# Kernel tuning notes

Hardware: AMD Instinct MI355X
Metric: run time of the kernel (lower is better)

## Reference

```python
import jax, jax.numpy as jnp
import numpy as np

B, S, HID = 2, 2048, 2048
NH, NKV, HD = 16, 4, 128
G = NH // NKV  # kv group size
EPS = 1e-6


def setup_inputs() -> dict:
    key = jax.random.key(0)
    ks = jax.random.split(key, 7)
    w = 0.02
    return {
        "hidden_states": jax.random.normal(ks[0], (B, S, HID), dtype=jnp.float32),
        "position_ids": jnp.broadcast_to(jnp.arange(S, dtype=jnp.int64), (B, S)),
        "Wq": jax.random.normal(ks[1], (2 * NH * HD, HID), dtype=jnp.float32) * w,
        "Wk": jax.random.normal(ks[2], (NKV * HD, HID), dtype=jnp.float32) * w,
        "Wv": jax.random.normal(ks[3], (NKV * HD, HID), dtype=jnp.float32) * w,
        "Wo": jax.random.normal(ks[4], (HID, NH * HD), dtype=jnp.float32) * w,
        "norm_w": jnp.zeros((HID,), dtype=jnp.float32),
    }


def reference(hidden_states, position_ids, Wq, Wk, Wv, Wo, norm_w):
    # RMSNorm (weight parameterized as 1 + w, per source)
    ms = jnp.mean(hidden_states * hidden_states, axis=-1, keepdims=True)
    x = hidden_states * jax.lax.rsqrt(ms + EPS) * (1.0 + norm_w)

    qg = x @ Wq.T                                   # (B,S,2*NH*HD)
    q, gate = jnp.split(qg, 2, axis=-1)
    q = q.reshape(B, S, NH, HD).transpose(0, 2, 1, 3)       # (B,NH,S,HD)
    gate = gate.reshape(B, S, NH, HD).transpose(0, 2, 1, 3)
    k = (x @ Wk.T).reshape(B, S, NKV, HD).transpose(0, 2, 1, 3)  # (B,NKV,S,HD)
    v = (x @ Wv.T).reshape(B, S, NKV, HD).transpose(0, 2, 1, 3)

    scale = 1.0 / np.sqrt(HD).astype(np.float32)
    qg4 = q.reshape(B, NKV, G, S, HD)
    attn = jnp.einsum("bkgqd,bkld->bkgql", qg4, k) * scale   # (B,NKV,G,S,S)
    p = jax.nn.softmax(attn, axis=-1)
    o = jnp.einsum("bkgql,bkld->bkgqd", p, v).reshape(B, NH, S, HD)

    o = o * jax.nn.sigmoid(gate)                    # output gate
    o = o.transpose(0, 2, 1, 3).reshape(B, S, NH * HD)
    return o @ Wo.T
```

## Files before the change

kernel.cpp:

```cpp
#include <hip/hip_runtime.h>
#include <math.h>

#define BB    2
#define SS    2048
#define HIDD  2048
#define NHH   16
#define NKVV  4
#define HDD   128
#define MROWS 4096
#define QG_N  4096
#define KV_N  512
#define O_N   2048
#define KDIM  2048
#define EPS_  1e-6f
#define SCALE_ 0.08838834764831845f
#define SCALE2_ (0.08838834764831845f * 1.4426950408889634f)
#define THR2_  11.5417f
#define NWBLK 14336

typedef __attribute__((ext_vector_type(8))) __bf16 bf16x8;
typedef __attribute__((ext_vector_type(8))) unsigned short u16x8;
typedef __attribute__((ext_vector_type(4))) float f32x4;

__device__ __forceinline__ unsigned short f2bf(float f) {
  return __builtin_bit_cast(unsigned short, (__bf16)f);
}
__device__ __forceinline__ float fexp2(float x) {
  return __builtin_amdgcn_exp2f(x);
}

__global__ __launch_bounds__(256) void prep_k(const float* __restrict__ Wq,
                                              const float* __restrict__ Wk,
                                              const float* __restrict__ Wv,
                                              const float* __restrict__ Wo,
                                              const float* __restrict__ hs,
                                              const float* __restrict__ nw,
                                              unsigned short* __restrict__ wdst,
                                              unsigned short* __restrict__ x) {
  if (blockIdx.x < NWBLK) {
    const int s0 = QG_N * KDIM / 4;
    const int s1 = s0 + KV_N * KDIM / 4;
    const int s2 = s1 + KV_N * KDIM / 4;
    int i = blockIdx.x * 256 + threadIdx.x;
    float4 v;
    if (i < s0)      v = ((const float4*)Wq)[i];
    else if (i < s1) v = ((const float4*)Wk)[i - s0];
    else if (i < s2) v = ((const float4*)Wv)[i - s1];
    else             v = ((const float4*)Wo)[i - s2];
    ushort4 u;
    u.x = f2bf(v.x); u.y = f2bf(v.y); u.z = f2bf(v.z); u.w = f2bf(v.w);
    ((ushort4*)wdst)[i] = u;
    return;
  }
  int row = blockIdx.x - NWBLK;
  int t = threadIdx.x;
  const float4* hr = (const float4*)(hs + (size_t)row * HIDD);
  const float4* w4 = (const float4*)nw;

  float4 v0 = hr[t], v1 = hr[t + 256];
  float ss = v0.x*v0.x + v0.y*v0.y + v0.z*v0.z + v0.w*v0.w
           + v1.x*v1.x + v1.y*v1.y + v1.z*v1.z + v1.w*v1.w;
#pragma unroll
  for (int off = 32; off > 0; off >>= 1) ss += __shfl_down(ss, off, 64);

  __shared__ float part[4];
  __shared__ float rs_sh;
  if ((t & 63) == 0) part[t >> 6] = ss;
  __syncthreads();
  if (t == 0) rs_sh = rsqrtf((part[0]+part[1]+part[2]+part[3]) * (1.0f/HIDD) + EPS_);
  __syncthreads();
  float rs = rs_sh;

  float4 w0 = w4[t], w1 = w4[t + 256];
  ushort4 o0, o1;
  o0.x = f2bf(v0.x * rs * (1.f + w0.x));
  o0.y = f2bf(v0.y * rs * (1.f + w0.y));
  o0.z = f2bf(v0.z * rs * (1.f + w0.z));
  o0.w = f2bf(v0.w * rs * (1.f + w0.w));
  o1.x = f2bf(v1.x * rs * (1.f + w1.x));
  o1.y = f2bf(v1.y * rs * (1.f + w1.y));
  o1.z = f2bf(v1.z * rs * (1.f + w1.z));
  o1.w = f2bf(v1.w * rs * (1.f + w1.w));
  ushort4* xr = (ushort4*)(x + (size_t)row * HIDD);
  xr[t] = o0;
  xr[t + 256] = o1;
}

template <int OBF>
__device__ __forceinline__ void gemm_core(const unsigned short* __restrict__ Ab,
                                          const unsigned short* __restrict__ Bb,
                                          void* __restrict__ Cv,
                                          int Ndim, int bm, int bn,
                                          unsigned short* Als, unsigned short* Bls) {
  char* ldsA = (char*)Als;
  char* ldsB = (char*)Bls;

  int t   = threadIdx.x;
  int r15 = t & 15;
  int g   = (t & 63) >> 4;
  int w   = t >> 6;
  int wr  = w >> 1, wc = w & 1;

  f32x4 acc[4][4] = {};

  for (int k0 = 0; k0 < KDIM; k0 += 64) {
    __syncthreads();
#pragma unroll
    for (int it = 0; it < 4; ++it) {
      int f      = it * 256 + t;
      int row    = f >> 3;
      int schunk = (f & 7) ^ (row & 7);
      unsigned ldsbase = (unsigned)((it * 256 + (w << 6)) << 4);
      __builtin_amdgcn_global_load_lds(
          (const unsigned int*)(Ab + ((size_t)(bm + row) << 11) + k0 + schunk * 8),
          (unsigned int*)(ldsA + ldsbase), 16, 0, 0);
      __builtin_amdgcn_global_load_lds(
          (const unsigned int*)(Bb + ((size_t)(bn + row) << 11) + k0 + schunk * 8),
          (unsigned int*)(ldsB + ldsbase), 16, 0, 0);
    }
    __syncthreads();

#pragma unroll
    for (int tt = 0; tt < 2; ++tt) {
      bf16x8 af[4], bfv[4];
#pragma unroll
      for (int mi = 0; mi < 4; ++mi) {
        int row = wr * 64 + mi * 16 + r15;
        af[mi] = *(const bf16x8*)(ldsA + row * 128 + (((4 * tt + g) ^ (row & 7)) << 4));
      }
#pragma unroll
      for (int ni = 0; ni < 4; ++ni) {
        int row = wc * 64 + ni * 16 + r15;
        bfv[ni] = *(const bf16x8*)(ldsB + row * 128 + (((4 * tt + g) ^ (row & 7)) << 4));
      }
      __builtin_amdgcn_s_setprio(1);
#pragma unroll
      for (int mi = 0; mi < 4; ++mi)
#pragma unroll
        for (int ni = 0; ni < 4; ++ni)
          acc[mi][ni] = __builtin_amdgcn_mfma_f32_16x16x32_bf16(af[mi], bfv[ni], acc[mi][ni], 0, 0, 0);
      __builtin_amdgcn_s_setprio(0);
    }
  }

#pragma unroll
  for (int mi = 0; mi < 4; ++mi)
#pragma unroll
    for (int ni = 0; ni < 4; ++ni) {
      int col = bn + wc * 64 + ni * 16 + r15;
#pragma unroll
      for (int r = 0; r < 4; ++r) {
        int rowg = bm + wr * 64 + mi * 16 + g * 4 + r;
        if (OBF == 1)
          ((unsigned short*)Cv)[(size_t)rowg * Ndim + col] = f2bf(acc[mi][ni][r]);
        else if (OBF == 3) {
          int t6 = rowg & 63;
          int sig = (t6 & 32) + ((t6 & 12) << 1) + ((t6 & 16) >> 2) + (t6 & 3);
          int tokp = (rowg & ~63) | sig;
          ((unsigned short*)Cv)[(size_t)col * MROWS + tokp] = f2bf(acc[mi][ni][r]);
        } else
          ((float*)Cv)[(size_t)rowg * Ndim + col] = acc[mi][ni][r];
      }
    }
}

__global__ __launch_bounds__(256) void gemm_kv(const unsigned short* __restrict__ Ab,
                                               const unsigned short* __restrict__ Wk,
                                               const unsigned short* __restrict__ Wv,
                                               unsigned short* __restrict__ Ck,
                                               unsigned short* __restrict__ Cvt) {
  __shared__ unsigned short Als[128 * 64];
  __shared__ unsigned short Bls[128 * 64];
  int bx = blockIdx.x;
  if (bx < 4)
    gemm_core<1>(Ab, Wk, (void*)Ck, KV_N, blockIdx.y * 128, bx * 128, Als, Bls);
  else
    gemm_core<3>(Ab, Wv, (void*)Cvt, KV_N, blockIdx.y * 128, (bx & 3) * 128, Als, Bls);
}

#define LD8(basep, r, x) \
  (*(const bf16x8*)((basep) + (size_t)(r) * 128 + ((((x) ^ ((r)&7))) << 4)))

#define STAGE_A(bufi, h, tk)                                                   \
  { _Pragma("unroll")                                                          \
    for (int c = 0; c < 2; ++c) {                                              \
      int f = c * 512 + t;                                                     \
      int rr = f >> 3;                                                         \
      int sc = (f & 7) ^ (rr & 7);                                             \
      __builtin_amdgcn_global_load_lds(                                        \
        (const unsigned int*)(Ab + ((size_t)(bm + (h)*128 + rr) << 11) + (tk)*64 + sc*8), \
        (unsigned int*)(lds8 + (bufi)*32768 + (h)*16384 + c*8192 + (w<<10)), 16, 0, 0); \
    } }

#define STAGE_B(bufi, h, tk)                                                   \
  { _Pragma("unroll")                                                          \
    for (int c = 0; c < 2; ++c) {                                              \
      int f = c * 512 + t;                                                     \
      int rr = f >> 3;                                                         \
      int sc = (f & 7) ^ (rr & 7);                                             \
      __builtin_amdgcn_global_load_lds(                                        \
        (const unsigned int*)(Bbp + ((size_t)(bn + (h)*128 + rr) << 11) + (tk)*64 + sc*8), \
        (unsigned int*)(lds8 + 65536 + (bufi)*32768 + (h)*16384 + c*8192 + (w<<10)), 16, 0, 0); \
    } }

#define RD_A(SRC, MIBASE)                                                      \
  { _Pragma("unroll")                                                          \
    for (int mi = 0; mi < 4; ++mi) {                                           \
      int rr = wr * 128 + ((MIBASE) + mi) * 16 + r15;                          \
      afr[mi][0] = LD8(SRC, rr, g);                                            \
      afr[mi][1] = LD8(SRC, rr, 4 + g);                                        \
    } }

#define RD_B(SRC, NIBASE, DST)                                                 \
  { _Pragma("unroll")                                                          \
    for (int ni = 0; ni < 2; ++ni) {                                           \
      int rr = wc * 64 + ((NIBASE) + ni) * 16 + r15;                           \
      DST[ni][0] = LD8(SRC, rr, g);                                            \
      DST[ni][1] = LD8(SRC, rr, 4 + g);                                        \
    } }

#define MFMA_QUAD(MIBASE, NIBASE, BREG)                                        \
  { __builtin_amdgcn_s_setprio(1);                                             \
    _Pragma("unroll")                                                          \
    for (int mi = 0; mi < 4; ++mi)                                             \
      _Pragma("unroll")                                                        \
      for (int ni = 0; ni < 2; ++ni)                                           \
        _Pragma("unroll")                                                      \
        for (int ks = 0; ks < 2; ++ks)                                         \
          acc[(MIBASE)+mi][(NIBASE)+ni] =                                      \
            __builtin_amdgcn_mfma_f32_16x16x32_bf16(afr[mi][ks], BREG[ni][ks], \
                                                    acc[(MIBASE)+mi][(NIBASE)+ni], 0, 0, 0); \
    __builtin_amdgcn_s_setprio(0); }

#define BAR() __builtin_amdgcn_s_barrier()

__global__ __launch_bounds__(512, 2) void gemm_qg256(const unsigned short* __restrict__ Ab,
                                                     const unsigned short* __restrict__ Bbp,
                                                     unsigned short* __restrict__ Cq,
                                                     float* __restrict__ Cg) {
  __shared__ char lds8[131072];
  int t = threadIdx.x;
  int r15 = t & 15, g = (t & 63) >> 4, w = t >> 6;
  int wr = w >> 2, wc = w & 3;
  int bm = blockIdx.y * 256, bn = blockIdx.x * 256;
  char* A0 = lds8;            char* A1 = lds8 + 32768;
  char* B0 = lds8 + 65536;    char* B1 = lds8 + 98304;

  f32x4 acc[8][4] = {};
  bf16x8 afr[4][2], b0r[2][2], b1r[2][2];

  STAGE_A(0, 0, 0); STAGE_A(0, 1, 0); STAGE_B(0, 0, 0); STAGE_B(0, 1, 0);
  STAGE_A(1, 0, 1); STAGE_A(1, 1, 1); STAGE_B(1, 0, 1); STAGE_B(1, 1, 1);
  asm volatile("s_waitcnt vmcnt(8)" ::: "memory");
  BAR();

  for (int i = 0; i < 15; ++i) {
    int te = 2 * i + 2, to = 2 * i + 3;
    RD_A(A0, 0); RD_B(B0, 0, b0r);
    BAR(); MFMA_QUAD(0, 0, b0r); BAR();
    RD_B(B0, 2, b1r);
    BAR(); MFMA_QUAD(0, 2, b1r); BAR();
    RD_A(A0, 4);
    STAGE_B(0, 0, te);
    BAR(); MFMA_QUAD(4, 0, b0r); BAR();
    STAGE_A(0, 0, te);
    BAR(); MFMA_QUAD(4, 2, b1r);
    asm volatile("s_waitcnt vmcnt(4)" ::: "memory");
    BAR();
    RD_A(A1, 0); RD_B(B1, 0, b0r);
    STAGE_A(0, 1, te);
    BAR(); MFMA_QUAD(0, 0, b0r); BAR();
    RD_B(B1, 2, b1r);
    STAGE_B(0, 1, te);
    BAR(); MFMA_QUAD(0, 2, b1r); BAR();
    RD_A(A1, 4);
    STAGE_B(1, 0, to); STAGE_B(1, 1, to);
    BAR(); MFMA_QUAD(4, 0, b0r); BAR();
    STAGE_A(1, 0, to); STAGE_A(1, 1, to);
    BAR(); MFMA_QUAD(4, 2, b1r);
    asm volatile("s_waitcnt vmcnt(8)" ::: "memory");
    BAR();
  }
  RD_A(A0, 0); RD_B(B0, 0, b0r);
  BAR(); MFMA_QUAD(0, 0, b0r); BAR();
  RD_B(B0, 2, b1r);
  BAR(); MFMA_QUAD(0, 2, b1r); BAR();
  RD_A(A0, 4);
  BAR(); MFMA_QUAD(4, 0, b0r); BAR();
  BAR(); MFMA_QUAD(4, 2, b1r);
  asm volatile("s_waitcnt vmcnt(0)" ::: "memory");
  BAR();
  RD_A(A1, 0); RD_B(B1, 0, b0r);
  BAR(); MFMA_QUAD(0, 0, b0r); BAR();
  RD_B(B1, 2, b1r);
  BAR(); MFMA_QUAD(0, 2, b1r); BAR();
  RD_A(A1, 4);
  BAR(); MFMA_QUAD(4, 0, b0r); BAR();
  BAR(); MFMA_QUAD(4, 2, b1r);

  bool isq = (bn < O_N);
  int colbase = bn + wc * 64;
#pragma unroll
  for (int mi = 0; mi < 8; ++mi) {
    size_t row = (size_t)bm + wr * 128 + mi * 16 + g * 4;
#pragma unroll
    for (int ni = 0; ni < 4; ++ni) {
      int col = colbase + ni * 16 + r15;
#pragma unroll
      for (int r = 0; r < 4; ++r) {
        if (isq) Cq[(row + r) * O_N + col] = f2bf(acc[mi][ni][r] * SCALE2_);
        else     Cg[(row + r) * O_N + (col - O_N)] = acc[mi][ni][r];
      }
    }
  }
}

#define OST_A(bufi, h, tk)                                                     \
  { _Pragma("unroll")                                                          \
    for (int c = 0; c < 2; ++c) {                                              \
      int f = c * 512 + t;                                                     \
      int rr = f >> 3;                                                         \
      int sc = (f & 7) ^ (rr & 7);                                             \
      __builtin_amdgcn_global_load_lds(                                        \
        (const unsigned int*)(Ab + ((size_t)(bm + (h)*128 + rr) << 11) + (tk)*64 + sc*8), \
        (unsigned int*)(lds8 + (bufi)*32768 + (h)*16384 + c*8192 + (w<<10)), 16, 0, 0); \
    } }

#define OST_B(bufi, tk)                                                        \
  { _Pragma("unroll")                                                          \
    for (int c = 0; c < 2; ++c) {                                              \
      int f = c * 512 + t;                                                     \
      int rr = f >> 3;                                                         \
      int sc = (f & 7) ^ (rr & 7);                                             \
      __builtin_amdgcn_global_load_lds(                                        \
        (const unsigned int*)(Bbp + ((size_t)(bn + rr) << 11) + (tk)*64 + sc*8), \
        (unsigned int*)(lds8 + 65536 + (bufi)*16384 + c*8192 + (w<<10)), 16, 0, 0); \
    } }

#define ORD_A(bufi)                                                            \
  { const char* abase = lds8 + (bufi)*32768 + (wr >> 1)*16384;                 \
    _Pragma("unroll")                                                          \
    for (int mi = 0; mi < 4; ++mi) {                                           \
      int rl = ((wr & 1) * 64) + mi * 16 + r15;                                \
      afr[mi][0] = LD8(abase, rl, g);                                          \
      afr[mi][1] = LD8(abase, rl, 4 + g);                                      \
    } }

#define ORD_B(bufi, NIBASE, DST)                                               \
  { const char* bbase = lds8 + 65536 + (bufi)*16384;                           \
    _Pragma("unroll")                                                          \
    for (int ni = 0; ni < 2; ++ni) {                                           \
      int rl = wc * 64 + ((NIBASE) + ni) * 16 + r15;                           \
      DST[ni][0] = LD8(bbase, rl, g);                                          \
      DST[ni][1] = LD8(bbase, rl, 4 + g);                                      \
    } }

#define OMFMA(NIBASE, BREG)                                                    \
  { __builtin_amdgcn_s_setprio(1);                                             \
    _Pragma("unroll")                                                          \
    for (int mi = 0; mi < 4; ++mi)                                             \
      _Pragma("unroll")                                                        \
      for (int ni = 0; ni < 2; ++ni)                                           \
        _Pragma("unroll")                                                      \
        for (int ks = 0; ks < 2; ++ks)                                         \
          acc[mi][(NIBASE)+ni] =                                               \
            __builtin_amdgcn_mfma_f32_16x16x32_bf16(afr[mi][ks], BREG[ni][ks], \
                                                    acc[mi][(NIBASE)+ni], 0, 0, 0); \
    __builtin_amdgcn_s_setprio(0); }

__global__ __launch_bounds__(512, 2) void gemm_o256(const unsigned short* __restrict__ Ab,
                                                    const unsigned short* __restrict__ Bbp,
                                                    float* __restrict__ C) {
  __shared__ char lds8[98304];
  int t = threadIdx.x;
  int r15 = t & 15, g = (t & 63) >> 4, w = t >> 6;
  int wr = w >> 1, wc = w & 1;
  int bm = blockIdx.y * 256, bn = blockIdx.x * 128;

  f32x4 acc[4][4] = {};
  bf16x8 afr[4][2], b0r[2][2], b1r[2][2];

  OST_A(0, 0, 0); OST_A(0, 1, 0); OST_B(0, 0);
  OST_A(1, 0, 1); OST_A(1, 1, 1);
  asm volatile("s_waitcnt vmcnt(4)" ::: "memory");
  BAR();

  for (int i = 0; i < 15; ++i) {
    int to = 2 * i + 1, te2 = 2 * i + 2, to2 = 2 * i + 3;
    ORD_A(0); ORD_B(0, 0, b0r);
    OST_B(1, to);
    BAR(); OMFMA(0, b0r); BAR();
    ORD_B(0, 2, b1r);
    OST_A(0, 0, te2);
    BAR(); OMFMA(2, b1r);
    asm volatile("s_waitcnt vmcnt(2)" ::: "memory");
    BAR();
    ORD_A(1); ORD_B(1, 0, b0r);
    OST_A(0, 1, te2); OST_B(0, te2);
    BAR(); OMFMA(0, b0r); BAR();
    ORD_B(1, 2, b1r);
    OST_A(1, 0, to2); OST_A(1, 1, to2);
    BAR(); OMFMA(2, b1r);
    asm volatile("s_waitcnt vmcnt(4)" ::: "memory");
    BAR();
  }
  ORD_A(0); ORD_B(0, 0, b0r);
  OST_B(1, 31);
  BAR(); OMFMA(0, b0r); BAR();
  ORD_B(0, 2, b1r);
  BAR(); OMFMA(2, b1r);
  asm volatile("s_waitcnt vmcnt(0)" ::: "memory");
  BAR();
  ORD_A(1); ORD_B(1, 0, b0r);
  BAR(); OMFMA(0, b0r); BAR();
  ORD_B(1, 2, b1r);
  BAR(); OMFMA(2, b1r);

#pragma unroll
  for (int mi = 0; mi < 4; ++mi) {
    size_t row = (size_t)bm + wr * 64 + mi * 16 + g * 4;
#pragma unroll
    for (int ni = 0; ni < 4; ++ni) {
      int col = bn + wc * 64 + ni * 16 + r15;
#pragma unroll
      for (int r = 0; r < 4; ++r)
        C[(row + r) * O_N + col] = acc[mi][ni][r];
    }
  }
}

__global__ __launch_bounds__(256, 2) void attn_mfma(const unsigned short* __restrict__ qb,
                                                    const float* __restrict__ gateb,
                                                    const unsigned short* __restrict__ kb,
                                                    const unsigned short* __restrict__ vt,
                                                    unsigned short* __restrict__ obuf) {
  __shared__ unsigned short Ks[2][64 * 128];
  __shared__ unsigned short Vt[2][128 * 64];
  char* ldsK0 = (char*)Ks;
  char* ldsV0 = (char*)Vt;

  int t = threadIdx.x;
  int l = t & 63, w = t >> 6;
  int c15 = l & 15, g = l >> 4;
  int bid = blockIdx.x;
  int swz = (bid & 7) * 64 + (bid >> 3);
  int qt = swz & 15, h = (swz >> 4) & 15, b = swz >> 8;
  int kh = h >> 2;
  size_t rowQ0 = (size_t)b * SS + (size_t)qt * 128;
  size_t rowKbase = (size_t)b * SS;

  bf16x8 qf[2][4];
#pragma unroll
  for (int qi = 0; qi < 2; ++qi)
#pragma unroll
    for (int ks = 0; ks < 4; ++ks)
      qf[qi][ks] = *(const bf16x8*)(qb + (rowQ0 + w * 32 + qi * 16 + c15) * O_N
                                       + h * HDD + g * 8 + ks * 32);

  f32x4 accO[2][8] = {};
  float mrun[2] = {-INFINITY, -INFINITY};
  float lrun[2] = {0.f, 0.f};

#define ISSUE_K(bufi, kt_)                                                     \
  {                                                                            \
    size_t rowK0 = rowKbase + (size_t)(kt_) * 64;                              \
    _Pragma("unroll")                                                          \
    for (int it = 0; it < 4; ++it) {                                           \
      int f = it * 256 + t;                                                    \
      int kv = f >> 4;                                                         \
      int schunk = (f & 15) ^ (kv & 7);                                        \
      unsigned ldsbase = (unsigned)((it * 256 + (w << 6)) << 4);               \
      __builtin_amdgcn_global_load_lds(                                        \
          (const unsigned int*)(kb + (rowK0 + kv) * KV_N + kh * HDD + schunk * 8), \
          (unsigned int*)(ldsK0 + (bufi) * 16384 + ldsbase), 16, 0, 0);        \
    }                                                                          \
  }
#define ISSUE_VT(bufi, kt_)                                                    \
  {                                                                            \
    size_t tokbase = rowKbase + (size_t)(kt_) * 64;                            \
    _Pragma("unroll")                                                          \
    for (int it = 0; it < 4; ++it) {                                           \
      int f = it * 256 + t;                                                    \
      int row = f >> 3;                                                        \
      int schunk = (f & 7) ^ (row & 7);                                        \
      unsigned ldsbase = (unsigned)((it * 256 + (w << 6)) << 4);               \
      __builtin_amdgcn_global_load_lds(                                        \
          (const unsigned int*)(vt + (size_t)(kh * 128 + row) * MROWS + tokbase + schunk * 8), \
          (unsigned int*)(ldsV0 + (bufi) * 16384 + ldsbase), 16, 0, 0);        \
    }                                                                          \
  }

  ISSUE_K(0, 0);
  ISSUE_VT(0, 0);
  asm volatile("s_waitcnt vmcnt(0)" ::: "memory");
  __syncthreads();

  const int NT = SS / 64;
  for (int kt = 0; kt < NT; ++kt) {
    int cur = kt & 1, nxt = cur ^ 1;
    char* ldsK = ldsK0 + cur * 16384;
    char* ldsV = ldsV0 + cur * 16384;

    if (kt + 1 < NT) {
      ISSUE_K(nxt, kt + 1);
      ISSUE_VT(nxt, kt + 1);
    }

    f32x4 accS[2][4] = {};
    __builtin_amdgcn_s_setprio(1);
#pragma unroll
    for (int nf = 0; nf < 4; ++nf) {
      int kvr = nf * 16 + c15;
#pragma unroll
      for (int ks = 0; ks < 4; ++ks) {
        bf16x8 kf = *(const bf16x8*)(ldsK + kvr * 256 + ((((g + 4 * ks) ^ (kvr & 7)) << 4)));
#pragma unroll
        for (int qi = 0; qi < 2; ++qi)
          accS[qi][nf] = __builtin_amdgcn_mfma_f32_16x16x32_bf16(kf, qf[qi][ks], accS[qi][nf], 0, 0, 0);
      }
    }
    __builtin_amdgcn_s_setprio(0);

    float mt[2];
#pragma unroll
    for (int qi = 0; qi < 2; ++qi) {
      float m0 = fmaxf(fmaxf(accS[qi][0][0], accS[qi][0][1]), fmaxf(accS[qi][0][2], accS[qi][0][3]));
#pragma unroll
      for (int nf = 1; nf < 4; ++nf)
        m0 = fmaxf(m0, fmaxf(fmaxf(accS[qi][nf][0], accS[qi][nf][1]), fmaxf(accS[qi][nf][2], accS[qi][nf][3])));
      m0 = fmaxf(m0, __shfl_xor(m0, 16, 64));
      m0 = fmaxf(m0, __shfl_xor(m0, 32, 64));
      mt[qi] = m0;
    }

    bool safe = (mt[0] <= mrun[0] + THR2_) && (mt[1] <= mrun[1] + THR2_);
    if (!__all(safe)) {
#pragma unroll
      for (int qi = 0; qi < 2; ++qi) {
        float mnew = fmaxf(mrun[qi], mt[qi]);
        float al = fexp2(mrun[qi] - mnew);
        mrun[qi] = mnew;
        lrun[qi] *= al;
        float alr[4];
#pragma unroll
        for (int r = 0; r < 4; ++r) alr[r] = __shfl(al, g * 4 + r, 16);
#pragma unroll
        for (int df = 0; df < 8; ++df)
#pragma unroll
          for (int r = 0; r < 4; ++r) accO[qi][df][r] *= alr[r];
      }
    }

    u16x8 pfr[2][2];
#pragma unroll
    for (int qi = 0; qi < 2; ++qi) {
      float ps = 0.f;
#pragma unroll
      for (int nf = 0; nf < 4; ++nf) {
        float p0 = fexp2(accS[qi][nf][0] - mrun[qi]);
        float p1 = fexp2(accS[qi][nf][1] - mrun[qi]);
        float p2 = fexp2(accS[qi][nf][2] - mrun[qi]);
        float p3 = fexp2(accS[qi][nf][3] - mrun[qi]);
        ps += (p0 + p1) + (p2 + p3);
        pfr[qi][nf >> 1][(nf & 1) * 4 + 0] = f2bf(p0);
        pfr[qi][nf >> 1][(nf & 1) * 4 + 1] = f2bf(p1);
        pfr[qi][nf >> 1][(nf & 1) * 4 + 2] = f2bf(p2);
        pfr[qi][nf >> 1][(nf & 1) * 4 + 3] = f2bf(p3);
      }
      lrun[qi] += ps;
    }

    __builtin_amdgcn_s_setprio(1);
#pragma unroll
    for (int ks2 = 0; ks2 < 2; ++ks2) {
      bf16x8 pf0 = __builtin_bit_cast(bf16x8, pfr[0][ks2]);
      bf16x8 pf1 = __builtin_bit_cast(bf16x8, pfr[1][ks2]);
#pragma unroll
      for (int df = 0; df < 8; ++df) {
        int d = df * 16 + c15;
        bf16x8 vf = *(const bf16x8*)(ldsV + d * 128 + ((((g + 4 * ks2) ^ (d & 7)) << 4)));
        accO[0][df] = __builtin_amdgcn_mfma_f32_16x16x32_bf16(pf0, vf, accO[0][df], 0, 0, 0);
        accO[1][df] = __builtin_amdgcn_mfma_f32_16x16x32_bf16(pf1, vf, accO[1][df], 0, 0, 0);
      }
    }
    __builtin_amdgcn_s_setprio(0);

    if (kt + 1 < NT) {
      asm volatile("s_waitcnt vmcnt(0)" ::: "memory");
    }
    __syncthreads();
  }

#pragma unroll
  for (int qi = 0; qi < 2; ++qi) {
    lrun[qi] += __shfl_xor(lrun[qi], 16, 64);
    lrun[qi] += __shfl_xor(lrun[qi], 32, 64);
    float invL = 1.f / lrun[qi];
    float ivr[4];
#pragma unroll
    for (int r = 0; r < 4; ++r) ivr[r] = __shfl(invL, g * 4 + r, 16);
#pragma unroll
    for (int r = 0; r < 4; ++r) {
      size_t row = rowQ0 + w * 32 + qi * 16 + g * 4 + r;
#pragma unroll
      for (int df = 0; df < 8; ++df) {
        int d = df * 16 + c15;
        float gt = gateb[row * (size_t)O_N + h * HDD + d];
        float sg = 1.f / (1.f + __expf(-gt));
        obuf[row * (size_t)O_N + h * HDD + d] = f2bf(accO[qi][df][r] * ivr[r] * sg);
      }
    }
  }
#undef ISSUE_K
#undef ISSUE_VT
}

extern "C" void kernel_launch(void* const* d_in, const int* in_sizes, int n_in,
                              void* d_out, int out_size, void* d_ws, size_t ws_size,
                              hipStream_t stream) {
  const float* hs = (const float*)d_in[0];
  const float* Wq = (const float*)d_in[2];
  const float* Wk = (const float*)d_in[3];
  const float* Wv = (const float*)d_in[4];
  const float* Wo = (const float*)d_in[5];
  const float* nw = (const float*)d_in[6];
  float* out = (float*)d_out;

  float* gateb = (float*)d_ws;
  unsigned short* qb16 = (unsigned short*)(gateb + (size_t)MROWS * O_N);
  unsigned short* kb16 = qb16 + (size_t)MROWS * O_N;
  unsigned short* vt16 = kb16 + (size_t)MROWS * KV_N;
  unsigned short* xb   = vt16 + (size_t)KV_N * MROWS;
  unsigned short* ob   = xb   + (size_t)MROWS * HIDD;
  unsigned short* wqb  = ob   + (size_t)MROWS * O_N;
  unsigned short* wkb  = wqb  + (size_t)QG_N * KDIM;
  unsigned short* wvb  = wkb  + (size_t)KV_N * KDIM;
  unsigned short* wob  = wvb  + (size_t)KV_N * KDIM;

  prep_k<<<dim3(NWBLK + MROWS), 256, 0, stream>>>(Wq, Wk, Wv, Wo, hs, nw, wqb, xb);

  gemm_qg256<<<dim3(QG_N/256, MROWS/256), 512, 0, stream>>>(xb, wqb, qb16, gateb);
  gemm_kv<<<dim3(8, MROWS/128), 256, 0, stream>>>(xb, wkb, wvb, kb16, vt16);
  attn_mfma<<<dim3(512), 256, 0, stream>>>(qb16, gateb, kb16, vt16, ob);
  gemm_o256<<<dim3(O_N/128, MROWS/256), 512, 0, stream>>>(ob, wob, out);
}
```

Before: 245.2 us.

## Software-pipeline attention loop: overlap next QK^T with current softmax and PV

Restructures the flash-attention inner loop so the QK^T MFMAs for the next key tile are interleaved with the exp/pack of the current tile, followed by the PV MFMAs. K moves to a triple buffer and the tile loop is unrolled by six to handle the buffer rotation. vmcnt waits become partial so loads stay in flight across iterations. The aim is to hide softmax VALU latency and memory waits behind matrix work, at the cost of more registers, more LDS and harder-to-verify buffer indexing.

```diff
diff --git a/kernel.cpp b/kernel.cpp
--- a/kernel.cpp
+++ b/kernel.cpp
@@ -434,7 +434,7 @@
                                                     const unsigned short* __restrict__ kb,
                                                     const unsigned short* __restrict__ vt,
                                                     unsigned short* __restrict__ obuf) {
-  __shared__ unsigned short Ks[2][64 * 128];
+  __shared__ unsigned short Ks[3][64 * 128];
   __shared__ unsigned short Vt[2][128 * 64];
   char* ldsK0 = (char*)Ks;
   char* ldsV0 = (char*)Vt;
@@ -458,6 +458,7 @@
                                        + h * HDD + g * 8 + ks * 32);
 
   f32x4 accO[2][8] = {};
+  f32x4 accA[2][4], accB[2][4];
   float mrun[2] = {-INFINITY, -INFINITY};
   float lrun[2] = {0.f, 0.f};
 
@@ -489,107 +490,129 @@
           (unsigned int*)(ldsV0 + (bufi) * 16384 + ldsbase), 16, 0, 0);        \
     }                                                                          \
   }
-
-  ISSUE_K(0, 0);
-  ISSUE_VT(0, 0);
-  asm volatile("s_waitcnt vmcnt(0)" ::: "memory");
+#define QKT_NF(NXT, KRD, NF)                                                   \
+  { int kvr = (NF) * 16 + c15;                                                 \
+    _Pragma("unroll")                                                          \
+    for (int ks = 0; ks < 4; ++ks) {                                           \
+      bf16x8 kf = *(const bf16x8*)(ldsK0 + (KRD) * 16384 + kvr * 256 +         \
+                                   ((((g + 4 * ks) ^ (kvr & 7)) << 4)));       \
+      NXT[0][NF] = __builtin_amdgcn_mfma_f32_16x16x32_bf16(kf, qf[0][ks], NXT[0][NF], 0, 0, 0); \
+      NXT[1][NF] = __builtin_amdgcn_mfma_f32_16x16x32_bf16(kf, qf[1][ks], NXT[1][NF], 0, 0, 0); \
+    } }
+#define MAXRESC(CUR)                                                           \
+  { float mtv[2];                                                              \
+    _Pragma("unroll")                                                          \
+    for (int qi = 0; qi < 2; ++qi) {                                           \
+      float m0 = fmaxf(fmaxf(CUR[qi][0][0], CUR[qi][0][1]),                    \
+                       fmaxf(CUR[qi][0][2], CUR[qi][0][3]));                   \
+      _Pragma("unroll")                                                        \
+      for (int nf = 1; nf < 4; ++nf)                                           \
+        m0 = fmaxf(m0, fmaxf(fmaxf(CUR[qi][nf][0], CUR[qi][nf][1]),            \
+                             fmaxf(CUR[qi][nf][2], CUR[qi][nf][3])));          \
+      m0 = fmaxf(m0, __shfl_xor(m0, 16, 64));                                  \
+      m0 = fmaxf(m0, __shfl_xor(m0, 32, 64));                                  \
+      mtv[qi] = m0;                                                            \
+    }                                                                          \
+    bool safe = (mtv[0] <= mrun[0] + THR2_) && (mtv[1] <= mrun[1] + THR2_);    \
+    if (!__all(safe)) {                                                        \
+      _Pragma("unroll")                                                        \
+      for (int qi = 0; qi < 2; ++qi) {                                         \
+        float mnew = fmaxf(mrun[qi], mtv[qi]);                                 \
+        float al = fexp2(mrun[qi] - mnew);                                     \
+        mrun[qi] = mnew;                                                       \
+        lrun[qi] *= al;                                                        \
+        float alr[4];                                                          \
+        _Pragma("unroll")                                                      \
+        for (int r = 0; r < 4; ++r) alr[r] = __shfl(al, g * 4 + r, 16);        \
+        _Pragma("unroll")                                                      \
+        for (int df = 0; df < 8; ++df)                                         \
+          _Pragma("unroll")                                                    \
+          for (int r = 0; r < 4; ++r) accO[qi][df][r] *= alr[r];               \
+      }                                                                        \
+    }                                                                          \
+  }
+#define EXPPACK_NF(CUR, NF)                                                    \
+  { float a0 = fexp2(CUR[0][NF][0] - mrun[0]);                                 \
+    float a1 = fexp2(CUR[0][NF][1] - mrun[0]);                                 \
+    float a2 = fexp2(CUR[0][NF][2] - mrun[0]);                                 \
+    float a3 = fexp2(CUR[0][NF][3] - mrun[0]);                                 \
+    ps0 += (a0 + a1) + (a2 + a3);                                              \
+    pfr[0][(NF) >> 1][((NF) & 1) * 4 + 0] = f2bf(a0);                          \
+    pfr[0][(NF) >> 1][((NF) & 1) * 4 + 1] = f2bf(a1);                          \
+    pfr[0][(NF) >> 1][((NF) & 1) * 4 + 2] = f2bf(a2);                          \
+    pfr[0][(NF) >> 1][((NF) & 1) * 4 + 3] = f2bf(a3);                          \
+    float b0 = fexp2(CUR[1][NF][0] - mrun[1]);                                 \
+    float b1 = fexp2(CUR[1][NF][1] - mrun[1]);                                 \
+    float b2 = fexp2(CUR[1][NF][2] - mrun[1]);                                 \
+    float b3 = fexp2(CUR[1][NF][3] - mrun[1]);                                 \
+    ps1 += (b0 + b1) + (b2 + b3);                                              \
+    pfr[1][(NF) >> 1][((NF) & 1) * 4 + 0] = f2bf(b0);                          \
+    pfr[1][(NF) >> 1][((NF) & 1) * 4 + 1] = f2bf(b1);                          \
+    pfr[1][(NF) >> 1][((NF) & 1) * 4 + 2] = f2bf(b2);                          \
+    pfr[1][(NF) >> 1][((NF) & 1) * 4 + 3] = f2bf(b3);                          \
+  }
+#define PV_BLOCK(VBUF)                                                         \
+  { _Pragma("unroll")                                                          \
+    for (int ks2 = 0; ks2 < 2; ++ks2) {                                        \
+      bf16x8 pf0 = __builtin_bit_cast(bf16x8, pfr[0][ks2]);                    \
+      bf16x8 pf1 = __builtin_bit_cast(bf16x8, pfr[1][ks2]);                    \
+      _Pragma("unroll")                                                        \
+      for (int df = 0; df < 8; ++df) {                                         \
+        int d = df * 16 + c15;                                                 \
+        bf16x8 vf = *(const bf16x8*)(ldsV0 + (VBUF) * 16384 + d * 128 +        \
+                                     ((((g + 4 * ks2) ^ (d & 7)) << 4)));      \
+        accO[0][df] = __builtin_amdgcn_mfma_f32_16x16x32_bf16(pf0, vf, accO[0][df], 0, 0, 0); \
+        accO[1][df] = __builtin_amdgcn_mfma_f32_16x16x32_bf16(pf1, vf, accO[1][df], 0, 0, 0); \
+      }                                                                        \
+    } }
+#define ABODY(CUR, NXT, KRD, KISS, VBUF, TISS, WAITN, HN, HKI, HVI)            \
+  {                                                                            \
+    if (HKI) { ISSUE_K(KISS, TISS); }                                          \
+    MAXRESC(CUR);                                                              \
+    asm volatile("s_waitcnt vmcnt(" #WAITN ")" ::: "memory");                  \
+    __syncthreads();                                                           \
+    u16x8 pfr[2][2];                                                           \
+    float ps0 = 0.f, ps1 = 0.f;                                                \
+    if (HN) {                                                                  \
+      _Pragma("unroll")                                                        \
+      for (int qi = 0; qi < 2; ++qi)                                           \
+        _Pragma("unroll")                                                      \
+        for (int nf = 0; nf < 4; ++nf)                                         \
+          NXT[qi][nf] = (f32x4){0.f, 0.f, 0.f, 0.f};                           \
+    }                                                                          \
+    __builtin_amdgcn_s_setprio(1);                                             \
+    EXPPACK_NF(CUR, 0); if (HN) { QKT_NF(NXT, KRD, 0); }                       \
+    EXPPACK_NF(CUR, 1); if (HN) { QKT_NF(NXT, KRD, 1); }                       \
+    EXPPACK_NF(CUR, 2); if (HN) { QKT_NF(NXT, KRD, 2); }                       \
+    EXPPACK_NF(CUR, 3); if (HN) { QKT_NF(NXT, KRD, 3); }                       \
+    PV_BLOCK(VBUF);                                                            \
+    __builtin_amdgcn_s_setprio(0);                                             \
+    lrun[0] += ps0; lrun[1] += ps1;                                            \
+    __syncthreads();                                                           \
+    if (HVI) { ISSUE_VT(VBUF, TISS); }                                         \
+  }
+
+  ISSUE_K(0, 0); ISSUE_VT(0, 0);
+  ISSUE_K(1, 1); ISSUE_VT(1, 1);
+  asm volatile("s_waitcnt vmcnt(12)" ::: "memory");
   __syncthreads();
-
-  const int NT = SS / 64;
-  for (int kt = 0; kt < NT; ++kt) {
-    int cur = kt & 1, nxt = cur ^ 1;
-    char* ldsK = ldsK0 + cur * 16384;
-    char* ldsV = ldsV0 + cur * 16384;
-
-    if (kt + 1 < NT) {
-      ISSUE_K(nxt, kt + 1);
-      ISSUE_VT(nxt, kt + 1);
-    }
-
-    f32x4 accS[2][4] = {};
-    __builtin_amdgcn_s_setprio(1);
-#pragma unroll
-    for (int nf = 0; nf < 4; ++nf) {
-      int kvr = nf * 16 + c15;
-#pragma unroll
-      for (int ks = 0; ks < 4; ++ks) {
-        bf16x8 kf = *(const bf16x8*)(ldsK + kvr * 256 + ((((g + 4 * ks) ^ (kvr & 7)) << 4)));
-#pragma unroll
-        for (int qi = 0; qi < 2; ++qi)
-          accS[qi][nf] = __builtin_amdgcn_mfma_f32_16x16x32_bf16(kf, qf[qi][ks], accS[qi][nf], 0, 0, 0);
-      }
-    }
-    __builtin_amdgcn_s_setprio(0);
-
-    float mt[2];
-#pragma unroll
-    for (int qi = 0; qi < 2; ++qi) {
-      float m0 = fmaxf(fmaxf(accS[qi][0][0], accS[qi][0][1]), fmaxf(accS[qi][0][2], accS[qi][0][3]));
-#pragma unroll
-      for (int nf = 1; nf < 4; ++nf)
-        m0 = fmaxf(m0, fmaxf(fmaxf(accS[qi][nf][0], accS[qi][nf][1]), fmaxf(accS[qi][nf][2], accS[qi][nf][3])));
-      m0 = fmaxf(m0, __shfl_xor(m0, 16, 64));
-      m0 = fmaxf(m0, __shfl_xor(m0, 32, 64));
-      mt[qi] = m0;
-    }
-
-    bool safe = (mt[0] <= mrun[0] + THR2_) && (mt[1] <= mrun[1] + THR2_);
-    if (!__all(safe)) {
-#pragma unroll
-      for (int qi = 0; qi < 2; ++qi) {
-        float mnew = fmaxf(mrun[qi], mt[qi]);
-        float al = fexp2(mrun[qi] - mnew);
-        mrun[qi] = mnew;
-        lrun[qi] *= al;
-        float alr[4];
-#pragma unroll
-        for (int r = 0; r < 4; ++r) alr[r] = __shfl(al, g * 4 + r, 16);
-#pragma unroll
-        for (int df = 0; df < 8; ++df)
-#pragma unroll
-          for (int r = 0; r < 4; ++r) accO[qi][df][r] *= alr[r];
-      }
-    }
-
-    u16x8 pfr[2][2];
-#pragma unroll
-    for (int qi = 0; qi < 2; ++qi) {
-      float ps = 0.f;
-#pragma unroll
-      for (int nf = 0; nf < 4; ++nf) {
-        float p0 = fexp2(accS[qi][nf][0] - mrun[qi]);
-        float p1 = fexp2(accS[qi][nf][1] - mrun[qi]);
-        float p2 = fexp2(accS[qi][nf][2] - mrun[qi]);
-        float p3 = fexp2(accS[qi][nf][3] - mrun[qi]);
-        ps += (p0 + p1) + (p2 + p3);
-        pfr[qi][nf >> 1][(nf & 1) * 4 + 0] = f2bf(p0);
-        pfr[qi][nf >> 1][(nf & 1) * 4 + 1] = f2bf(p1);
-        pfr[qi][nf >> 1][(nf & 1) * 4 + 2] = f2bf(p2);
-        pfr[qi][nf >> 1][(nf & 1) * 4 + 3] = f2bf(p3);
-      }
-      lrun[qi] += ps;
-    }
-
-    __builtin_amdgcn_s_setprio(1);
-#pragma unroll
-    for (int ks2 = 0; ks2 < 2; ++ks2) {
-      bf16x8 pf0 = __builtin_bit_cast(bf16x8, pfr[0][ks2]);
-      bf16x8 pf1 = __builtin_bit_cast(bf16x8, pfr[1][ks2]);
-#pragma unroll
-      for (int df = 0; df < 8; ++df) {
-        int d = df * 16 + c15;
-        bf16x8 vf = *(const bf16x8*)(ldsV + d * 128 + ((((g + 4 * ks2) ^ (d & 7)) << 4)));
-        accO[0][df] = __builtin_amdgcn_mfma_f32_16x16x32_bf16(pf0, vf, accO[0][df], 0, 0, 0);
-        accO[1][df] = __builtin_amdgcn_mfma_f32_16x16x32_bf16(pf1, vf, accO[1][df], 0, 0, 0);
-      }
-    }
-    __builtin_amdgcn_s_setprio(0);
-
-    if (kt + 1 < NT) {
-      asm volatile("s_waitcnt vmcnt(0)" ::: "memory");
-    }
-    __syncthreads();
-  }
+#pragma unroll
+  for (int qi = 0; qi < 2; ++qi)
+#pragma unroll
+    for (int nf = 0; nf < 4; ++nf)
+      accA[qi][nf] = (f32x4){0.f, 0.f, 0.f, 0.f};
+  QKT_NF(accA, 0, 0); QKT_NF(accA, 0, 1); QKT_NF(accA, 0, 2); QKT_NF(accA, 0, 3);
+
+  for (int tb = 0; tb < 30; tb += 6) {
+    ABODY(accA, accB, 1, 2, 0, tb + 2, 8, 1, 1, 1);
+    ABODY(accB, accA, 2, 0, 1, tb + 3, 8, 1, 1, 1);
+    ABODY(accA, accB, 0, 1, 0, tb + 4, 8, 1, 1, 1);
+    ABODY(accB, accA, 1, 2, 1, tb + 5, 8, 1, 1, 1);
+    ABODY(accA, accB, 2, 0, 0, tb + 6, 8, 1, 1, 1);
+    ABODY(accB, accA, 0, 1, 1, tb + 7, 8, 1, 1, 1);
+  }
+  ABODY(accA, accB, 1, 0, 0, 32, 4, 1, 0, 0);
+  ABODY(accB, accA, 0, 0, 1, 32, 0, 0, 0, 0);
 
 #pragma unroll
   for (int qi = 0; qi < 2; ++qi) {
@@ -613,6 +636,11 @@
   }
 #undef ISSUE_K
 #undef ISSUE_VT
+#undef QKT_NF
+#undef MAXRESC
+#undef EXPPACK_NF
+#undef PV_BLOCK
+#undef ABODY
 }
 
 extern "C" void kernel_launch(void* const* d_in, const int* in_sizes, int n_in,
```

After: 290.3 us. +18.4%, slower.
